# Kernel optimization log

Measured on AMD Instinct MI355X. Metric: run time of the kernel, lower is better.

## Reference

```python
import jax, jax.numpy as jnp
import numpy as np

K = 20  # n_neighbors

def _edge_features(x, k):
    # x: [B, C, N] -> edge features [B, 2C, N, k] using dynamic kNN graph
    sq = jnp.sum(x * x, axis=1)                          # [B, N]
    inner = jnp.einsum('bcn,bcm->bnm', x, x)             # [B, N, N]
    neg_dist = 2.0 * inner - sq[:, :, None] - sq[:, None, :]
    idx = jax.lax.top_k(neg_dist, k)[1]                  # [B, N, k] nearest neighbors
    # gather neighbor features: xj[b,c,n,j] = x[b,c,idx[b,n,j]]
    xj = jnp.take_along_axis(x[:, :, None, :], idx[:, None, :, :], axis=3)  # [B, C, N, k]
    xi = jnp.broadcast_to(x[:, :, :, None], xj.shape)
    return jnp.concatenate([xj - xi, xi], axis=1)        # [B, 2C, N, k]

def _lrelu(v):
    return jax.nn.leaky_relu(v, 0.2)

def _edge_conv(x, W, b, k):
    f = _edge_features(x, k)                              # [B, 2C, N, k]
    h = jnp.einsum('bcnk,oc->bonk', f, W) + b[None, :, None, None]
    return jnp.max(_lrelu(h), axis=3)                     # [B, O, N]

def setup_inputs() -> dict:
    key = jax.random.key(0)
    ks = jax.random.split(key, 12)
    conv_dims = (64, 64, 128, 256)
    in_dims = (3, 64, 64, 128)
    inp = {'x': jax.random.normal(ks[0], (16, 2048, 3), dtype=jnp.float32)}
    for i, (ci, co) in enumerate(zip(in_dims, conv_dims)):
        s = 1.0 / np.sqrt(2 * ci)
        inp[f'W{i}'] = jax.random.uniform(ks[1 + 2 * i], (co, 2 * ci), jnp.float32, -s, s)
        inp[f'b{i}'] = jax.random.uniform(ks[2 + 2 * i], (co,), jnp.float32, -s, s)
    sf = 1.0 / np.sqrt(sum(conv_dims))
    inp['Wf'] = jax.random.uniform(ks[9], (1024, sum(conv_dims)), jnp.float32, -sf, sf)
    inp['bf'] = jax.random.uniform(ks[10], (1024,), jnp.float32, -sf, sf)
    return inp

def reference(x, W0, b0, W1, b1, W2, b2, W3, b3, Wf, bf):
    h = jnp.transpose(x, (0, 2, 1))                       # [B, 3, N]
    xs = []
    for W, b in ((W0, b0), (W1, b1), (W2, b2), (W3, b3)):
        h = _edge_conv(h, W, b, K)
        xs.append(h)
    h = jnp.concatenate(xs, axis=1)                       # [B, 512, N]
    h = _lrelu(jnp.einsum('bcn,oc->bon', h, Wf) + bf[None, :, None])  # [B, 1024, N]
    return jnp.max(h, axis=2)                             # [B, 1024]
```

## Files before the change

kernel.cpp:

```cpp
#include <hip/hip_runtime.h>
#include <hip/hip_bf16.h>
#include <math.h>

#define NPTS 2048
#define NB 16
#define KNN 20

typedef __attribute__((ext_vector_type(8))) short bf16x8;
typedef __attribute__((ext_vector_type(4))) float f32x4;

__device__ __forceinline__ float lrelu(float v) { return fmaxf(v, 0.2f * v); }

__device__ __forceinline__ void split2(float a, float b, unsigned& hp, unsigned& lp) {
    float2 f2; f2.x = a; f2.y = b;
    __hip_bfloat162 h2 = __float22bfloat162_rn(f2);
    unsigned hb; __builtin_memcpy(&hb, &h2, 4);
    float la = a - __uint_as_float(hb << 16);
    float lb = b - __uint_as_float(hb & 0xFFFF0000u);
    float2 l2; l2.x = la; l2.y = lb;
    __hip_bfloat162 k2 = __float22bfloat162_rn(l2);
    unsigned lb2; __builtin_memcpy(&lb2, &k2, 4);
    hp = hb; lp = lb2;
}

template<int CTRL, int RM>
__device__ __forceinline__ float dpp_fmax_step(float x) {
    int t = __builtin_amdgcn_update_dpp((int)0xFF800000, __float_as_int(x),
                                        CTRL, RM, 0xF, false);
    return fmaxf(x, __int_as_float(t));
}
__device__ __forceinline__ float wave_max_bcast(float x) {
    x = dpp_fmax_step<0x111, 0xF>(x);
    x = dpp_fmax_step<0x112, 0xF>(x);
    x = dpp_fmax_step<0x114, 0xF>(x);
    x = dpp_fmax_step<0x118, 0xF>(x);
    x = dpp_fmax_step<0x142, 0xA>(x);
    x = dpp_fmax_step<0x143, 0xC>(x);
    return __int_as_float(__builtin_amdgcn_readlane(__float_as_int(x), 63));
}

__global__ void transpose_kernel(const float* __restrict__ x, float* __restrict__ h0) {
    int t = blockIdx.x * blockDim.x + threadIdx.x;
    if (t >= NB * NPTS) return;
    int b = t / NPTS, n = t % NPTS;
    const float* src = x + (size_t)t * 3;
    float* dst = h0 + (size_t)b * 3 * NPTS + n;
    dst[0]        = src[0];
    dst[NPTS]     = src[1];
    dst[2 * NPTS] = src[2];
}

template<int C>
__global__ __launch_bounds__(512) void knn_kernel(const float* __restrict__ xin, long bstride,
                                                  int* __restrict__ idx) {
    __shared__ __align__(16) float dist[8][NPTS];
    int b = blockIdx.y;
    int n0 = blockIdx.x * 8;
    int tid = threadIdx.x;
    const float* xb = xin + (size_t)b * bstride;
    const float* xq = xb + n0;

    int m0 = 4 * tid;
    float4 acc[8];
#pragma unroll
    for (int r = 0; r < 8; ++r) acc[r] = make_float4(0.f, 0.f, 0.f, 0.f);
    float4 sn = make_float4(0.f, 0.f, 0.f, 0.f);

#pragma unroll 4
    for (int c = 0; c < C; ++c) {
        const float* rowc = xb + (size_t)c * NPTS;
        float4 xv = *reinterpret_cast<const float4*>(&rowc[m0]);
        float4 q0 = *reinterpret_cast<const float4*>(&xq[(size_t)c * NPTS]);
        float4 q1 = *reinterpret_cast<const float4*>(&xq[(size_t)c * NPTS + 4]);
        sn.x = fmaf(xv.x, xv.x, sn.x);
        sn.y = fmaf(xv.y, xv.y, sn.y);
        sn.z = fmaf(xv.z, xv.z, sn.z);
        sn.w = fmaf(xv.w, xv.w, sn.w);
        float q[8] = {q0.x, q0.y, q0.z, q0.w, q1.x, q1.y, q1.z, q1.w};
#pragma unroll
        for (int r = 0; r < 8; ++r) {
            acc[r].x = fmaf(q[r], xv.x, acc[r].x);
            acc[r].y = fmaf(q[r], xv.y, acc[r].y);
            acc[r].z = fmaf(q[r], xv.z, acc[r].z);
            acc[r].w = fmaf(q[r], xv.w, acc[r].w);
        }
    }
    {
        int p = m0 ^ (((m0 >> 5) & 7) << 2);
#pragma unroll
        for (int r = 0; r < 8; ++r) {
            float4 dv;
            dv.x = 2.f * acc[r].x - sn.x;
            dv.y = 2.f * acc[r].y - sn.y;
            dv.z = 2.f * acc[r].z - sn.z;
            dv.w = 2.f * acc[r].w - sn.w;
            *reinterpret_cast<float4*>(&dist[r][p]) = dv;
        }
    }
    __syncthreads();

    int w = tid >> 6;
    int lane = tid & 63;
    float v[32];
    {
        const float* drow = &dist[w][32 * lane];
        int s = (lane & 7) << 2;
#pragma unroll
        for (int u = 0; u < 8; ++u) {
            float4 t = *reinterpret_cast<const float4*>(&drow[(4 * u) ^ s]);
            v[4 * u + 0] = t.x; v[4 * u + 1] = t.y;
            v[4 * u + 2] = t.z; v[4 * u + 3] = t.w;
        }
    }

    float gm[4]; int gi[4];
#pragma unroll
    for (int g = 0; g < 4; ++g) {
        gm[g] = v[8 * g]; gi[g] = 8 * g;
#pragma unroll
        for (int i = 1; i < 8; ++i)
            if (v[8 * g + i] > gm[g]) { gm[g] = v[8 * g + i]; gi[g] = 8 * g + i; }
    }
    float lv = gm[0]; int lm = gi[0];
#pragma unroll
    for (int g = 1; g < 4; ++g) if (gm[g] > lv) { lv = gm[g]; lm = gi[g]; }

    int rbm = 0;
    int* out = idx + ((size_t)b * NPTS + n0 + w) * KNN;

    for (int j = 0; j < KNN; ++j) {
        float gv = wave_max_bcast(lv);
        unsigned long long mk = __ballot(lv == gv);
        int winner = (int)__builtin_ctzll(mk);
        int wm = __builtin_amdgcn_readlane(lm, winner);
        int bm = winner * 32 + wm;
        rbm = (lane == j) ? bm : rbm;

        bool iswin = (lane == winner);
        int g = wm >> 3, ii = wm & 7;
#pragma unroll
        for (int gq = 0; gq < 4; ++gq) {
            if (gq == g) {
#pragma unroll
                for (int i = 0; i < 8; ++i)
                    v[8 * gq + i] = (iswin && (ii == i)) ? -INFINITY : v[8 * gq + i];
                float nm = v[8 * gq]; int ni = 8 * gq;
#pragma unroll
                for (int i = 1; i < 8; ++i)
                    if (v[8 * gq + i] > nm) { nm = v[8 * gq + i]; ni = 8 * gq + i; }
                gm[gq] = iswin ? nm : gm[gq];
                gi[gq] = iswin ? ni : gi[gq];
            }
        }
        lv = gm[0]; lm = gi[0];
#pragma unroll
        for (int g2 = 1; g2 < 4; ++g2) if (gm[g2] > lv) { lv = gm[g2]; lm = gi[g2]; }
    }
    if (lane < KNN) out[lane] = rbm;
}

__global__ void prep_w_kernel(const float* __restrict__ W, int C, int O,
                              float* __restrict__ Wa, float* __restrict__ Wd) {
    int t = blockIdx.x * blockDim.x + threadIdx.x;
    if (t >= C * O) return;
    int c = t / O, o = t % O;
    float a = W[o * 2 * C + c];
    float d = W[o * 2 * C + C + c] - a;
    Wa[c * O + o] = a;
    Wd[c * O + o] = d;
}

__global__ __launch_bounds__(256) void edge_mm_kernel(const float* __restrict__ xin, long bstride,
                                                      int C, int O,
                                                      const float* __restrict__ Wa,
                                                      const float* __restrict__ Wd,
                                                      const float* __restrict__ bias,
                                                      float* __restrict__ y,
                                                      float* __restrict__ base, long base_bstride) {
    int m = blockIdx.x * 256 + threadIdx.x;
    int ngrp = O >> 3;
    int og = blockIdx.y % ngrp, b = blockIdx.y / ngrp;
    int o0 = og * 8;
    const float* xb = xin + (size_t)b * bstride + m;
    float a1[8], a2[8];
#pragma unroll
    for (int i = 0; i < 8; ++i) { a1[i] = 0.f; a2[i] = 0.f; }
#pragma unroll 2
    for (int c = 0; c < C; ++c) {
        float h = xb[(size_t)c * NPTS];
        const float* wa = Wa + c * O + o0;
        const float* wd = Wd + c * O + o0;
#pragma unroll
        for (int i = 0; i < 8; ++i) {
            a1[i] = fmaf(wa[i], h, a1[i]);
            a2[i] = fmaf(wd[i], h, a2[i]);
        }
    }
#pragma unroll
    for (int i = 0; i < 8; ++i) {
        y[((size_t)b * O + o0 + i) * NPTS + m] = a1[i];
        base[(size_t)b * base_bstride + (size_t)(o0 + i) * NPTS + m] = a2[i] + bias[o0 + i];
    }
}

__global__ __launch_bounds__(256) void gather_max_kernel(const float* __restrict__ y, int O,
                                                         const int* __restrict__ idx,
                                                         float* __restrict__ feat_slice,
                                                         long bstride) {
    __shared__ float yrow[NPTS];
    int o = blockIdx.x, b = blockIdx.y;
    const float* ysrc = y + ((size_t)b * O + o) * NPTS;
    for (int m = threadIdx.x; m < NPTS; m += 256) yrow[m] = ysrc[m];
    __syncthreads();
    float* fs = feat_slice + (size_t)b * bstride + (size_t)o * NPTS;
    const int* ib = idx + (size_t)b * NPTS * KNN;
    for (int s = 0; s < 8; ++s) {
        int n = threadIdx.x + 256 * s;
        const int* ip = ib + n * KNN;
        float mx = -INFINITY;
#pragma unroll
        for (int j = 0; j < KNN; ++j) mx = fmaxf(mx, yrow[ip[j]]);
        fs[n] = lrelu(mx + fs[n]);
    }
}

__global__ void wf_split_kernel(const float* __restrict__ Wf,
                                unsigned* __restrict__ Wfh, unsigned* __restrict__ Wfl) {
    int t = blockIdx.x * 256 + threadIdx.x;
    if (t >= 262144) return;
    unsigned h, l;
    split2(Wf[2 * t], Wf[2 * t + 1], h, l);
    Wfh[t] = h; Wfl[t] = l;
}

#define GP 40
__global__ __launch_bounds__(256) void final_gemm_mfma(
    const float* __restrict__ feat,
    const unsigned short* __restrict__ Wfh,
    const unsigned short* __restrict__ Wfl,
    float* __restrict__ pmax) {
    __shared__ __align__(16) unsigned short Ah[128 * GP];
    __shared__ __align__(16) unsigned short Al[128 * GP];
    __shared__ __align__(16) unsigned short Bh[128 * GP];
    __shared__ __align__(16) unsigned short Bl[128 * GP];

    int ot = blockIdx.x, nt = blockIdx.y, b = blockIdx.z;
    int o0 = ot * 128, n0 = nt * 128;
    int tid = threadIdx.x;
    int lane = tid & 63, w = tid >> 6;
    int wm = w & 1, wn = w >> 1;
    int l15 = lane & 15, q = lane >> 4;

    f32x4 acc[4][4];
#pragma unroll
    for (int mi = 0; mi < 4; ++mi)
#pragma unroll
        for (int ni = 0; ni < 4; ++ni) acc[mi][ni] = (f32x4)0.f;

    const float* fb = feat + (size_t)b * 512 * NPTS;

    int bn = tid & 127, kh = tid >> 7;

    for (int c0 = 0; c0 < 512; c0 += 32) {
#pragma unroll
        for (int p = 0; p < 2; ++p) {
            int e = p * 256 + tid;
            int r = e >> 2, qq = e & 3;
            size_t go = (size_t)(o0 + r) * 512 + c0 + qq * 8;
            *(uint4*)&Ah[r * GP + qq * 8] = *(const uint4*)(Wfh + go);
            *(uint4*)&Al[r * GP + qq * 8] = *(const uint4*)(Wfl + go);
        }
        {
            const float* src = fb + (size_t)(c0 + kh * 16) * NPTS + n0 + bn;
            float v[16];
#pragma unroll
            for (int j = 0; j < 16; ++j) v[j] = src[(size_t)j * NPTS];
            unsigned hw[8], lw[8];
#pragma unroll
            for (int p = 0; p < 8; ++p) split2(v[2 * p], v[2 * p + 1], hw[p], lw[p]);
            unsigned short* bh = &Bh[bn * GP + kh * 16];
            unsigned short* bl = &Bl[bn * GP + kh * 16];
            *(uint4*)(bh)     = make_uint4(hw[0], hw[1], hw[2], hw[3]);
            *(uint4*)(bh + 8) = make_uint4(hw[4], hw[5], hw[6], hw[7]);
            *(uint4*)(bl)     = make_uint4(lw[0], lw[1], lw[2], lw[3]);
            *(uint4*)(bl + 8) = make_uint4(lw[4], lw[5], lw[6], lw[7]);
        }
        __syncthreads();

        bf16x8 bhf[4], blf[4];
#pragma unroll
        for (int ni = 0; ni < 4; ++ni) {
            int row = wn * 64 + ni * 16 + l15;
            bhf[ni] = *(const bf16x8*)&Bh[row * GP + q * 8];
            blf[ni] = *(const bf16x8*)&Bl[row * GP + q * 8];
        }
#pragma unroll
        for (int mi = 0; mi < 4; ++mi) {
            int row = wm * 64 + mi * 16 + l15;
            bf16x8 ah = *(const bf16x8*)&Ah[row * GP + q * 8];
            bf16x8 al = *(const bf16x8*)&Al[row * GP + q * 8];
#pragma unroll
            for (int ni = 0; ni < 4; ++ni) {
                acc[mi][ni] = __builtin_amdgcn_mfma_f32_16x16x32_bf16(ah, bhf[ni], acc[mi][ni], 0, 0, 0);
                acc[mi][ni] = __builtin_amdgcn_mfma_f32_16x16x32_bf16(ah, blf[ni], acc[mi][ni], 0, 0, 0);
                acc[mi][ni] = __builtin_amdgcn_mfma_f32_16x16x32_bf16(al, bhf[ni], acc[mi][ni], 0, 0, 0);
            }
        }
        __syncthreads();
    }

    int slot = nt * 2 + wn;
#pragma unroll
    for (int mi = 0; mi < 4; ++mi) {
        float m4[4];
#pragma unroll
        for (int r = 0; r < 4; ++r) {
            float m = acc[mi][0][r];
            m = fmaxf(m, acc[mi][1][r]);
            m = fmaxf(m, acc[mi][2][r]);
            m = fmaxf(m, acc[mi][3][r]);
            m4[r] = m;
        }
#pragma unroll
        for (int off = 1; off < 16; off <<= 1) {
#pragma unroll
            for (int r = 0; r < 4; ++r)
                m4[r] = fmaxf(m4[r], __shfl_xor(m4[r], off, 16));
        }
        if (l15 == 0) {
            int mbase = o0 + wm * 64 + mi * 16 + q * 4;
#pragma unroll
            for (int r = 0; r < 4; ++r)
                pmax[((size_t)b * 1024 + mbase + r) * 32 + slot] = m4[r];
        }
    }
}

__global__ void final_reduce_kernel(const float* __restrict__ pmax,
                                    const float* __restrict__ bf,
                                    float* __restrict__ out) {
    int t = blockIdx.x * blockDim.x + threadIdx.x;
    if (t >= NB * 1024) return;
    const float* p = pmax + (size_t)t * 32;
    float m = p[0];
#pragma unroll
    for (int i = 1; i < 32; ++i) m = fmaxf(m, p[i]);
    out[t] = lrelu(m + bf[t & 1023]);
}

extern "C" void kernel_launch(void* const* d_in, const int* in_sizes, int n_in,
                              void* d_out, int out_size, void* d_ws, size_t ws_size,
                              hipStream_t stream) {
    const float* x  = (const float*)d_in[0];
    const float* W[4]  = {(const float*)d_in[1], (const float*)d_in[3],
                          (const float*)d_in[5], (const float*)d_in[7]};
    const float* bb[4] = {(const float*)d_in[2], (const float*)d_in[4],
                          (const float*)d_in[6], (const float*)d_in[8]};
    const float* Wf = (const float*)d_in[9];
    const float* bf = (const float*)d_in[10];
    float* out = (float*)d_out;

    float* ws   = (float*)d_ws;
    float* h0   = ws;
    int*   idx  = (int*)(ws + 98304 + 32768);
    float* y    = (float*)(idx + 655360);
    float* feat = y + 8388608;
    float* Wa   = feat + 16777216 + 262144;
    float* Wd   = Wa + 32768;

    unsigned* Wfh = (unsigned*)y;
    unsigned* Wfl = (unsigned*)(y + 262144);
    float*    pmax = y + 524288;

    transpose_kernel<<<128, 256, 0, stream>>>(x, h0);

    const int  Cs[4]   = {3, 64, 64, 128};
    const int  Os[4]   = {64, 64, 128, 256};
    const int  offs[4] = {0, 64, 128, 256};

    for (int l = 0; l < 4; ++l) {
        const float* in = (l == 0) ? h0 : feat + (size_t)offs[l - 1] * NPTS;
        long bstr = (l == 0) ? (long)3 * NPTS : (long)512 * NPTS;
        int C = Cs[l], O = Os[l];

        dim3 kg(NPTS / 8, NB);
        if (C == 3)       knn_kernel<3>  <<<kg, 512, 0, stream>>>(in, bstr, idx);
        else if (C == 64) knn_kernel<64> <<<kg, 512, 0, stream>>>(in, bstr, idx);
        else              knn_kernel<128><<<kg, 512, 0, stream>>>(in, bstr, idx);

        prep_w_kernel<<<(C * O + 255) / 256, 256, 0, stream>>>(W[l], C, O, Wa, Wd);

        float* fslice = feat + (size_t)offs[l] * NPTS;
        edge_mm_kernel<<<dim3(NPTS / 256, NB * (O >> 3)), 256, 0, stream>>>(
            in, bstr, C, O, Wa, Wd, bb[l], y, fslice, (long)512 * NPTS);

        gather_max_kernel<<<dim3(O, NB), 256, 0, stream>>>(y, O, idx, fslice, (long)512 * NPTS);
    }

    wf_split_kernel<<<1024, 256, 0, stream>>>(Wf, Wfh, Wfl);
    final_gemm_mfma<<<dim3(8, 16, NB), 256, 0, stream>>>(
        feat, (const unsigned short*)Wfh, (const unsigned short*)Wfl, pmax);
    final_reduce_kernel<<<64, 256, 0, stream>>>(pmax, bf, out);
}
```

Before: 1.154 ms.

## Transpose kNN index layout and shrink kNN blocks to four query rows

The kNN kernel now uses 256-thread blocks that each handle 4 query points, with every thread computing 8 candidate distances instead of 4. Neighbor indices are stored transposed as [B, K, N] rather than [B, N, K]. With that layout, the gather-max kernel's per-neighbor index loads are coalesced across threads instead of strided by K. The smaller blocks halve shared memory per block and double the grid size, but reload the candidate rows twice as often per query.

```diff
diff --git a/kernel.cpp b/kernel.cpp
--- a/kernel.cpp
+++ b/kernel.cpp
@@ -51,50 +51,69 @@
 }
 
 template<int C>
-__global__ __launch_bounds__(512) void knn_kernel(const float* __restrict__ xin, long bstride,
-                                                  int* __restrict__ idx) {
-    __shared__ __align__(16) float dist[8][NPTS];
+__global__ __launch_bounds__(256) void knn_kernel(const float* __restrict__ xin, long bstride,
+                                                  int* __restrict__ idxT) {
+    __shared__ __align__(16) float dist[4][NPTS];
     int b = blockIdx.y;
-    int n0 = blockIdx.x * 8;
+    int n0 = blockIdx.x * 4;
     int tid = threadIdx.x;
     const float* xb = xin + (size_t)b * bstride;
     const float* xq = xb + n0;
 
-    int m0 = 4 * tid;
-    float4 acc[8];
-#pragma unroll
-    for (int r = 0; r < 8; ++r) acc[r] = make_float4(0.f, 0.f, 0.f, 0.f);
-    float4 sn = make_float4(0.f, 0.f, 0.f, 0.f);
+    int m0 = 8 * tid;
+    float4 acc[4][2];
+#pragma unroll
+    for (int r = 0; r < 4; ++r)
+#pragma unroll
+        for (int h = 0; h < 2; ++h) acc[r][h] = make_float4(0.f, 0.f, 0.f, 0.f);
+    float4 sn[2];
+    sn[0] = make_float4(0.f, 0.f, 0.f, 0.f);
+    sn[1] = make_float4(0.f, 0.f, 0.f, 0.f);
 
 #pragma unroll 4
     for (int c = 0; c < C; ++c) {
         const float* rowc = xb + (size_t)c * NPTS;
-        float4 xv = *reinterpret_cast<const float4*>(&rowc[m0]);
-        float4 q0 = *reinterpret_cast<const float4*>(&xq[(size_t)c * NPTS]);
-        float4 q1 = *reinterpret_cast<const float4*>(&xq[(size_t)c * NPTS + 4]);
-        sn.x = fmaf(xv.x, xv.x, sn.x);
-        sn.y = fmaf(xv.y, xv.y, sn.y);
-        sn.z = fmaf(xv.z, xv.z, sn.z);
-        sn.w = fmaf(xv.w, xv.w, sn.w);
-        float q[8] = {q0.x, q0.y, q0.z, q0.w, q1.x, q1.y, q1.z, q1.w};
-#pragma unroll
-        for (int r = 0; r < 8; ++r) {
-            acc[r].x = fmaf(q[r], xv.x, acc[r].x);
-            acc[r].y = fmaf(q[r], xv.y, acc[r].y);
-            acc[r].z = fmaf(q[r], xv.z, acc[r].z);
-            acc[r].w = fmaf(q[r], xv.w, acc[r].w);
+        float4 xv0 = *reinterpret_cast<const float4*>(&rowc[m0]);
+        float4 xv1 = *reinterpret_cast<const float4*>(&rowc[m0 + 4]);
+        float4 qv  = *reinterpret_cast<const float4*>(&xq[(size_t)c * NPTS]);
+        sn[0].x = fmaf(xv0.x, xv0.x, sn[0].x);
+        sn[0].y = fmaf(xv0.y, xv0.y, sn[0].y);
+        sn[0].z = fmaf(xv0.z, xv0.z, sn[0].z);
+        sn[0].w = fmaf(xv0.w, xv0.w, sn[0].w);
+        sn[1].x = fmaf(xv1.x, xv1.x, sn[1].x);
+        sn[1].y = fmaf(xv1.y, xv1.y, sn[1].y);
+        sn[1].z = fmaf(xv1.z, xv1.z, sn[1].z);
+        sn[1].w = fmaf(xv1.w, xv1.w, sn[1].w);
+        float q[4] = {qv.x, qv.y, qv.z, qv.w};
+#pragma unroll
+        for (int r = 0; r < 4; ++r) {
+            acc[r][0].x = fmaf(q[r], xv0.x, acc[r][0].x);
+            acc[r][0].y = fmaf(q[r], xv0.y, acc[r][0].y);
+            acc[r][0].z = fmaf(q[r], xv0.z, acc[r][0].z);
+            acc[r][0].w = fmaf(q[r], xv0.w, acc[r][0].w);
+            acc[r][1].x = fmaf(q[r], xv1.x, acc[r][1].x);
+            acc[r][1].y = fmaf(q[r], xv1.y, acc[r][1].y);
+            acc[r][1].z = fmaf(q[r], xv1.z, acc[r][1].z);
+            acc[r][1].w = fmaf(q[r], xv1.w, acc[r][1].w);
         }
     }
     {
-        int p = m0 ^ (((m0 >> 5) & 7) << 2);
-#pragma unroll
-        for (int r = 0; r < 8; ++r) {
-            float4 dv;
-            dv.x = 2.f * acc[r].x - sn.x;
-            dv.y = 2.f * acc[r].y - sn.y;
-            dv.z = 2.f * acc[r].z - sn.z;
-            dv.w = 2.f * acc[r].w - sn.w;
-            *reinterpret_cast<float4*>(&dist[r][p]) = dv;
+        int sw = ((m0 >> 5) & 7) << 2;
+        int p0 = m0 ^ sw;
+        int p1 = (m0 + 4) ^ sw;
+#pragma unroll
+        for (int r = 0; r < 4; ++r) {
+            float4 d0, d1;
+            d0.x = 2.f * acc[r][0].x - sn[0].x;
+            d0.y = 2.f * acc[r][0].y - sn[0].y;
+            d0.z = 2.f * acc[r][0].z - sn[0].z;
+            d0.w = 2.f * acc[r][0].w - sn[0].w;
+            d1.x = 2.f * acc[r][1].x - sn[1].x;
+            d1.y = 2.f * acc[r][1].y - sn[1].y;
+            d1.z = 2.f * acc[r][1].z - sn[1].z;
+            d1.w = 2.f * acc[r][1].w - sn[1].w;
+            *reinterpret_cast<float4*>(&dist[r][p0]) = d0;
+            *reinterpret_cast<float4*>(&dist[r][p1]) = d1;
         }
     }
     __syncthreads();
@@ -126,7 +145,6 @@
     for (int g = 1; g < 4; ++g) if (gm[g] > lv) { lv = gm[g]; lm = gi[g]; }
 
     int rbm = 0;
-    int* out = idx + ((size_t)b * NPTS + n0 + w) * KNN;
 
     for (int j = 0; j < KNN; ++j) {
         float gv = wave_max_bcast(lv);
@@ -156,7 +174,7 @@
 #pragma unroll
         for (int g2 = 1; g2 < 4; ++g2) if (gm[g2] > lv) { lv = gm[g2]; lm = gi[g2]; }
     }
-    if (lane < KNN) out[lane] = rbm;
+    if (lane < KNN) idxT[((size_t)b * KNN + lane) * NPTS + n0 + w] = rbm;
 }
 
 __global__ void prep_w_kernel(const float* __restrict__ W, int C, int O,
@@ -204,7 +222,7 @@
 }
 
 __global__ __launch_bounds__(256) void gather_max_kernel(const float* __restrict__ y, int O,
-                                                         const int* __restrict__ idx,
+                                                         const int* __restrict__ idxT,
                                                          float* __restrict__ feat_slice,
                                                          long bstride) {
     __shared__ float yrow[NPTS];
@@ -213,13 +231,12 @@
     for (int m = threadIdx.x; m < NPTS; m += 256) yrow[m] = ysrc[m];
     __syncthreads();
     float* fs = feat_slice + (size_t)b * bstride + (size_t)o * NPTS;
-    const int* ib = idx + (size_t)b * NPTS * KNN;
+    const int* ib = idxT + (size_t)b * KNN * NPTS;
     for (int s = 0; s < 8; ++s) {
         int n = threadIdx.x + 256 * s;
-        const int* ip = ib + n * KNN;
         float mx = -INFINITY;
 #pragma unroll
-        for (int j = 0; j < KNN; ++j) mx = fmaxf(mx, yrow[ip[j]]);
+        for (int j = 0; j < KNN; ++j) mx = fmaxf(mx, yrow[ib[(size_t)j * NPTS + n]]);
         fs[n] = lrelu(mx + fs[n]);
     }
 }
@@ -362,8 +379,8 @@
 
     float* ws   = (float*)d_ws;
     float* h0   = ws;
-    int*   idx  = (int*)(ws + 98304 + 32768);
-    float* y    = (float*)(idx + 655360);
+    int*   idxT = (int*)(ws + 98304 + 32768);
+    float* y    = (float*)(idxT + 655360);
     float* feat = y + 8388608;
     float* Wa   = feat + 16777216 + 262144;
     float* Wd   = Wa + 32768;
@@ -383,10 +400,10 @@
         long bstr = (l == 0) ? (long)3 * NPTS : (long)512 * NPTS;
         int C = Cs[l], O = Os[l];
 
-        dim3 kg(NPTS / 8, NB);
-        if (C == 3)       knn_kernel<3>  <<<kg, 512, 0, stream>>>(in, bstr, idx);
-        else if (C == 64) knn_kernel<64> <<<kg, 512, 0, stream>>>(in, bstr, idx);
-        else              knn_kernel<128><<<kg, 512, 0, stream>>>(in, bstr, idx);
+        dim3 kg(NPTS / 4, NB);
+        if (C == 3)       knn_kernel<3>  <<<kg, 256, 0, stream>>>(in, bstr, idxT);
+        else if (C == 64) knn_kernel<64> <<<kg, 256, 0, stream>>>(in, bstr, idxT);
+        else              knn_kernel<128><<<kg, 256, 0, stream>>>(in, bstr, idxT);
 
         prep_w_kernel<<<(C * O + 255) / 256, 256, 0, stream>>>(W[l], C, O, Wa, Wd);
 
@@ -394,7 +411,7 @@
         edge_mm_kernel<<<dim3(NPTS / 256, NB * (O >> 3)), 256, 0, stream>>>(
             in, bstr, C, O, Wa, Wd, bb[l], y, fslice, (long)512 * NPTS);
 
-        gather_max_kernel<<<dim3(O, NB), 256, 0, stream>>>(y, O, idx, fslice, (long)512 * NPTS);
+        gather_max_kernel<<<dim3(O, NB), 256, 0, stream>>>(y, O, idxT, fslice, (long)512 * NPTS);
     }
 
     wf_split_kernel<<<1024, 256, 0, stream>>>(Wf, Wfh, Wfl);
```

Measured after the change: 1.236 ms. 1.07x slower.

## Compute kNN distances with bf16x3-split MFMA and two-pass top-k selection

Applied to the files above, without the earlier changes.

Replaces the FP32 FMA pairwise-distance kNN kernel with a pre-pass that splits each point's features into three bf16 parts plus squared norms, then a kernel that computes the inner products with six 16x16x32 bf16 MFMAs per chunk, recovering near-FP32 accuracy. Each block handles 16 query rows in two halves of 1024 candidates. It picks 20 candidates per half and merges them with a second wave-level selection. The index layout becomes transposed [B,K,N] so that gather_max reads are coalesced. This adds an extra split kernel and its memory traffic per layer, and the bf16 split could rarely change neighbor ordering on near ties.

```diff
diff --git a/kernel.cpp b/kernel.cpp
--- a/kernel.cpp
+++ b/kernel.cpp
@@ -10,6 +10,14 @@
 typedef __attribute__((ext_vector_type(4))) float f32x4;
 
 __device__ __forceinline__ float lrelu(float v) { return fmaxf(v, 0.2f * v); }
+
+__device__ __forceinline__ unsigned short bf16r(float a) {
+    __hip_bfloat16 h = __float2bfloat16(a);
+    unsigned short u; __builtin_memcpy(&u, &h, 2); return u;
+}
+__device__ __forceinline__ float bf2f(unsigned short u) {
+    unsigned v = (unsigned)u << 16; float f; __builtin_memcpy(&f, &v, 4); return f;
+}
 
 __device__ __forceinline__ void split2(float a, float b, unsigned& hp, unsigned& lp) {
     float2 f2; f2.x = a; f2.y = b;
@@ -50,113 +58,172 @@
     dst[2 * NPTS] = src[2];
 }
 
-template<int C>
-__global__ __launch_bounds__(512) void knn_kernel(const float* __restrict__ xin, long bstride,
-                                                  int* __restrict__ idx) {
-    __shared__ __align__(16) float dist[8][NPTS];
-    int b = blockIdx.y;
-    int n0 = blockIdx.x * 8;
-    int tid = threadIdx.x;
-    const float* xb = xin + (size_t)b * bstride;
-    const float* xq = xb + n0;
-
-    int m0 = 4 * tid;
-    float4 acc[8];
-#pragma unroll
-    for (int r = 0; r < 8; ++r) acc[r] = make_float4(0.f, 0.f, 0.f, 0.f);
-    float4 sn = make_float4(0.f, 0.f, 0.f, 0.f);
-
-#pragma unroll 4
-    for (int c = 0; c < C; ++c) {
-        const float* rowc = xb + (size_t)c * NPTS;
-        float4 xv = *reinterpret_cast<const float4*>(&rowc[m0]);
-        float4 q0 = *reinterpret_cast<const float4*>(&xq[(size_t)c * NPTS]);
-        float4 q1 = *reinterpret_cast<const float4*>(&xq[(size_t)c * NPTS + 4]);
-        sn.x = fmaf(xv.x, xv.x, sn.x);
-        sn.y = fmaf(xv.y, xv.y, sn.y);
-        sn.z = fmaf(xv.z, xv.z, sn.z);
-        sn.w = fmaf(xv.w, xv.w, sn.w);
-        float q[8] = {q0.x, q0.y, q0.z, q0.w, q1.x, q1.y, q1.z, q1.w};
-#pragma unroll
-        for (int r = 0; r < 8; ++r) {
-            acc[r].x = fmaf(q[r], xv.x, acc[r].x);
-            acc[r].y = fmaf(q[r], xv.y, acc[r].y);
-            acc[r].z = fmaf(q[r], xv.z, acc[r].z);
-            acc[r].w = fmaf(q[r], xv.w, acc[r].w);
-        }
-    }
+template<int C, int CP>
+__global__ __launch_bounds__(256) void split_sq_kernel(const float* __restrict__ in, long bstride,
+                                                       unsigned short* __restrict__ xs,
+                                                       float* __restrict__ sq) {
+    int t = blockIdx.x * 256 + threadIdx.x;
+    int b = t >> 11, n = t & 2047;
+    const float* p = in + (size_t)b * bstride + n;
+    unsigned short* o = xs + (size_t)t * 3 * CP;
+    float s = 0.f;
+    for (int c0 = 0; c0 < CP; c0 += 4) {
+        unsigned short hh[4], mm[4], ll[4];
+#pragma unroll
+        for (int i = 0; i < 4; ++i) {
+            int c = c0 + i;
+            float a = (c < C) ? p[(size_t)c * NPTS] : 0.f;
+            if (c < C) s = fmaf(a, a, s);
+            unsigned short h = bf16r(a);
+            float r1 = a - bf2f(h);
+            unsigned short m = bf16r(r1);
+            float r2 = r1 - bf2f(m);
+            unsigned short l = bf16r(r2);
+            hh[i] = h; mm[i] = m; ll[i] = l;
+        }
+        *(uint2*)(o + 0 * CP + c0) = make_uint2((unsigned)hh[0] | ((unsigned)hh[1] << 16),
+                                                (unsigned)hh[2] | ((unsigned)hh[3] << 16));
+        *(uint2*)(o + 1 * CP + c0) = make_uint2((unsigned)mm[0] | ((unsigned)mm[1] << 16),
+                                                (unsigned)mm[2] | ((unsigned)mm[3] << 16));
+        *(uint2*)(o + 2 * CP + c0) = make_uint2((unsigned)ll[0] | ((unsigned)ll[1] << 16),
+                                                (unsigned)ll[2] | ((unsigned)ll[3] << 16));
+    }
+    sq[t] = s;
+}
+
+template<int CP>
+__global__ __launch_bounds__(512) void knn_mfma_kernel(const unsigned short* __restrict__ xs,
+                                                       const float* __restrict__ sq,
+                                                       int* __restrict__ idxT) {
+    __shared__ __align__(16) float dist[16 * 1024];
+    constexpr int KC = CP / 32;
+    int b = blockIdx.y, n0 = blockIdx.x * 16;
+    int tid = threadIdx.x, lane = tid & 63, w = tid >> 6;
+    int l15 = lane & 15, q = lane >> 4;
+
+    bf16x8 af[KC][3];
     {
-        int p = m0 ^ (((m0 >> 5) & 7) << 2);
-#pragma unroll
-        for (int r = 0; r < 8; ++r) {
-            float4 dv;
-            dv.x = 2.f * acc[r].x - sn.x;
-            dv.y = 2.f * acc[r].y - sn.y;
-            dv.z = 2.f * acc[r].z - sn.z;
-            dv.w = 2.f * acc[r].w - sn.w;
-            *reinterpret_cast<float4*>(&dist[r][p]) = dv;
-        }
-    }
-    __syncthreads();
-
-    int w = tid >> 6;
-    int lane = tid & 63;
-    float v[32];
-    {
-        const float* drow = &dist[w][32 * lane];
-        int s = (lane & 7) << 2;
-#pragma unroll
-        for (int u = 0; u < 8; ++u) {
-            float4 t = *reinterpret_cast<const float4*>(&drow[(4 * u) ^ s]);
-            v[4 * u + 0] = t.x; v[4 * u + 1] = t.y;
-            v[4 * u + 2] = t.z; v[4 * u + 3] = t.w;
-        }
-    }
-
-    float gm[4]; int gi[4];
-#pragma unroll
-    for (int g = 0; g < 4; ++g) {
-        gm[g] = v[8 * g]; gi[g] = 8 * g;
-#pragma unroll
-        for (int i = 1; i < 8; ++i)
-            if (v[8 * g + i] > gm[g]) { gm[g] = v[8 * g + i]; gi[g] = 8 * g + i; }
-    }
-    float lv = gm[0]; int lm = gi[0];
-#pragma unroll
-    for (int g = 1; g < 4; ++g) if (gm[g] > lv) { lv = gm[g]; lm = gi[g]; }
-
-    int rbm = 0;
-    int* out = idx + ((size_t)b * NPTS + n0 + w) * KNN;
-
-    for (int j = 0; j < KNN; ++j) {
-        float gv = wave_max_bcast(lv);
-        unsigned long long mk = __ballot(lv == gv);
-        int winner = (int)__builtin_ctzll(mk);
-        int wm = __builtin_amdgcn_readlane(lm, winner);
-        int bm = winner * 32 + wm;
-        rbm = (lane == j) ? bm : rbm;
-
-        bool iswin = (lane == winner);
-        int g = wm >> 3, ii = wm & 7;
-#pragma unroll
-        for (int gq = 0; gq < 4; ++gq) {
-            if (gq == g) {
-#pragma unroll
-                for (int i = 0; i < 8; ++i)
-                    v[8 * gq + i] = (iswin && (ii == i)) ? -INFINITY : v[8 * gq + i];
-                float nm = v[8 * gq]; int ni = 8 * gq;
-#pragma unroll
-                for (int i = 1; i < 8; ++i)
-                    if (v[8 * gq + i] > nm) { nm = v[8 * gq + i]; ni = 8 * gq + i; }
-                gm[gq] = iswin ? nm : gm[gq];
-                gi[gq] = iswin ? ni : gi[gq];
-            }
-        }
-        lv = gm[0]; lm = gi[0];
-#pragma unroll
-        for (int g2 = 1; g2 < 4; ++g2) if (gm[g2] > lv) { lv = gm[g2]; lm = gi[g2]; }
-    }
-    if (lane < KNN) out[lane] = rbm;
+        const unsigned short* ab = xs + ((size_t)b * NPTS + n0 + l15) * 3 * CP + q * 8;
+#pragma unroll
+        for (int kc = 0; kc < KC; ++kc)
+#pragma unroll
+            for (int cp = 0; cp < 3; ++cp)
+                af[kc][cp] = *(const bf16x8*)(ab + (size_t)cp * CP + kc * 32);
+    }
+    const float* sqb = sq + (size_t)b * NPTS;
+
+    float avalr[2]; int aidxr[2];
+    avalr[0] = avalr[1] = 0.f; aidxr[0] = aidxr[1] = 0;
+
+    for (int half = 0; half < 2; ++half) {
+        int chalf = half * 1024;
+        int lcb0 = w * 128;
+#pragma unroll 2
+        for (int t8 = 0; t8 < 8; ++t8) {
+            int lcb = lcb0 + t8 * 16;
+            int gc = chalf + lcb + l15;
+            const unsigned short* bb = xs + ((size_t)b * NPTS + gc) * 3 * CP + q * 8;
+            f32x4 acc = (f32x4)0.f;
+#pragma unroll
+            for (int kc = 0; kc < KC; ++kc) {
+                bf16x8 bh = *(const bf16x8*)(bb + 0 * CP + kc * 32);
+                bf16x8 bm = *(const bf16x8*)(bb + 1 * CP + kc * 32);
+                bf16x8 bl = *(const bf16x8*)(bb + 2 * CP + kc * 32);
+                acc = __builtin_amdgcn_mfma_f32_16x16x32_bf16(af[kc][1], bm, acc, 0, 0, 0);
+                acc = __builtin_amdgcn_mfma_f32_16x16x32_bf16(af[kc][0], bl, acc, 0, 0, 0);
+                acc = __builtin_amdgcn_mfma_f32_16x16x32_bf16(af[kc][2], bh, acc, 0, 0, 0);
+                acc = __builtin_amdgcn_mfma_f32_16x16x32_bf16(af[kc][0], bm, acc, 0, 0, 0);
+                acc = __builtin_amdgcn_mfma_f32_16x16x32_bf16(af[kc][1], bh, acc, 0, 0, 0);
+                acc = __builtin_amdgcn_mfma_f32_16x16x32_bf16(af[kc][0], bh, acc, 0, 0, 0);
+            }
+            float sv = sqb[gc];
+            int lc = lcb + l15;
+            int pc = lc ^ (((lc >> 5) & 7) << 2);
+#pragma unroll
+            for (int j = 0; j < 4; ++j) {
+                int r = q * 4 + j;
+                dist[r * 1024 + ((pc + 4 * r) & 1023)] = 2.f * acc[j] - sv;
+            }
+        }
+        __syncthreads();
+
+        int swl = ((lane >> 1) & 7) << 2;
+        for (int rs = 0; rs < 2; ++rs) {
+            int r = w + 8 * rs;
+            float v[16];
+#pragma unroll
+            for (int u = 0; u < 4; ++u) {
+                int lcl = (16 * lane + 4 * u) ^ swl;
+                const float4 tv = *(const float4*)&dist[r * 1024 + ((lcl + 4 * r) & 1023)];
+                v[4 * u + 0] = tv.x; v[4 * u + 1] = tv.y;
+                v[4 * u + 2] = tv.z; v[4 * u + 3] = tv.w;
+            }
+            float gm0 = v[0]; int gi0 = 0;
+            float gm1 = v[8]; int gi1 = 8;
+#pragma unroll
+            for (int i = 1; i < 8; ++i) {
+                if (v[i] > gm0) { gm0 = v[i]; gi0 = i; }
+                if (v[8 + i] > gm1) { gm1 = v[8 + i]; gi1 = 8 + i; }
+            }
+            float lv = gm0; int lm = gi0;
+            if (gm1 > lv) { lv = gm1; lm = gi1; }
+
+            float cv = -INFINITY; int ci = 0;
+            for (int j = 0; j < KNN; ++j) {
+                float gv = wave_max_bcast(lv);
+                unsigned long long mk = __ballot(lv == gv);
+                int winner = (int)__builtin_ctzll(mk);
+                int wm = __builtin_amdgcn_readlane(lm, winner);
+                int bm = chalf + winner * 16 + wm;
+                cv = (lane == j) ? gv : cv;
+                ci = (lane == j) ? bm : ci;
+                bool iswin = (lane == winner);
+                if ((wm >> 3) == 0) {
+#pragma unroll
+                    for (int i = 0; i < 8; ++i)
+                        v[i] = (iswin && (wm == i)) ? -INFINITY : v[i];
+                    float nm = v[0]; int ni = 0;
+#pragma unroll
+                    for (int i = 1; i < 8; ++i) if (v[i] > nm) { nm = v[i]; ni = i; }
+                    gm0 = iswin ? nm : gm0;
+                    gi0 = iswin ? ni : gi0;
+                } else {
+#pragma unroll
+                    for (int i = 8; i < 16; ++i)
+                        v[i] = (iswin && (wm == i)) ? -INFINITY : v[i];
+                    float nm = v[8]; int ni = 8;
+#pragma unroll
+                    for (int i = 9; i < 16; ++i) if (v[i] > nm) { nm = v[i]; ni = i; }
+                    gm1 = iswin ? nm : gm1;
+                    gi1 = iswin ? ni : gi1;
+                }
+                lv = gm0; lm = gi0;
+                if (gm1 > lv) { lv = gm1; lm = gi1; }
+            }
+
+            if (half == 0) { avalr[rs] = cv; aidxr[rs] = ci; }
+            else {
+                int src = (lane >= 32) ? (lane - 32) : 0;
+                float bsv = __shfl(cv, src, 64);
+                int   bsi = __shfl(ci, src, 64);
+                float mv; int mi2;
+                if (lane < 20)                    { mv = avalr[rs]; mi2 = aidxr[rs]; }
+                else if (lane >= 32 && lane < 52) { mv = bsv;       mi2 = bsi; }
+                else                              { mv = -INFINITY; mi2 = 0; }
+                int rbm = 0;
+                for (int j = 0; j < KNN; ++j) {
+                    float gv = wave_max_bcast(mv);
+                    unsigned long long mk = __ballot(mv == gv);
+                    int winner = (int)__builtin_ctzll(mk);
+                    int widx = __builtin_amdgcn_readlane(mi2, winner);
+                    rbm = (lane == j) ? widx : rbm;
+                    mv = (lane == winner) ? -INFINITY : mv;
+                }
+                if (lane < KNN) idxT[((size_t)b * KNN + lane) * NPTS + n0 + r] = rbm;
+            }
+        }
+        if (half == 0) __syncthreads();
+    }
 }
 
 __global__ void prep_w_kernel(const float* __restrict__ W, int C, int O,
@@ -204,7 +271,7 @@
 }
 
 __global__ __launch_bounds__(256) void gather_max_kernel(const float* __restrict__ y, int O,
-                                                         const int* __restrict__ idx,
+                                                         const int* __restrict__ idxT,
                                                          float* __restrict__ feat_slice,
                                                          long bstride) {
     __shared__ float yrow[NPTS];
@@ -213,13 +280,12 @@
     for (int m = threadIdx.x; m < NPTS; m += 256) yrow[m] = ysrc[m];
     __syncthreads();
     float* fs = feat_slice + (size_t)b * bstride + (size_t)o * NPTS;
-    const int* ib = idx + (size_t)b * NPTS * KNN;
+    const int* ib = idxT + (size_t)b * KNN * NPTS;
     for (int s = 0; s < 8; ++s) {
         int n = threadIdx.x + 256 * s;
-        const int* ip = ib + n * KNN;
         float mx = -INFINITY;
 #pragma unroll
-        for (int j = 0; j < KNN; ++j) mx = fmaxf(mx, yrow[ip[j]]);
+        for (int j = 0; j < KNN; ++j) mx = fmaxf(mx, yrow[ib[(size_t)j * NPTS + n]]);
         fs[n] = lrelu(mx + fs[n]);
     }
 }
@@ -258,7 +324,6 @@
         for (int ni = 0; ni < 4; ++ni) acc[mi][ni] = (f32x4)0.f;
 
     const float* fb = feat + (size_t)b * 512 * NPTS;
-
     int bn = tid & 127, kh = tid >> 7;
 
     for (int c0 = 0; c0 < 512; c0 += 32) {
@@ -362,11 +427,14 @@
 
     float* ws   = (float*)d_ws;
     float* h0   = ws;
-    int*   idx  = (int*)(ws + 98304 + 32768);
-    float* y    = (float*)(idx + 655360);
+    float* sq   = ws + 98304;
+    int*   idxT = (int*)(sq + 32768);
+    float* y    = (float*)(idxT + 655360);
     float* feat = y + 8388608;
     float* Wa   = feat + 16777216 + 262144;
     float* Wd   = Wa + 32768;
+
+    unsigned short* xs = (unsigned short*)y;
 
     unsigned* Wfh = (unsigned*)y;
     unsigned* Wfl = (unsigned*)(y + 262144);
@@ -383,10 +451,17 @@
         long bstr = (l == 0) ? (long)3 * NPTS : (long)512 * NPTS;
         int C = Cs[l], O = Os[l];
 
-        dim3 kg(NPTS / 8, NB);
-        if (C == 3)       knn_kernel<3>  <<<kg, 512, 0, stream>>>(in, bstr, idx);
-        else if (C == 64) knn_kernel<64> <<<kg, 512, 0, stream>>>(in, bstr, idx);
-        else              knn_kernel<128><<<kg, 512, 0, stream>>>(in, bstr, idx);
+        dim3 kg(NPTS / 16, NB);
+        if (C == 3) {
+            split_sq_kernel<3, 32><<<128, 256, 0, stream>>>(in, bstr, xs, sq);
+            knn_mfma_kernel<32><<<kg, 512, 0, stream>>>(xs, sq, idxT);
+        } else if (C == 64) {
+            split_sq_kernel<64, 64><<<128, 256, 0, stream>>>(in, bstr, xs, sq);
+            knn_mfma_kernel<64><<<kg, 512, 0, stream>>>(xs, sq, idxT);
+        } else {
+            split_sq_kernel<128, 128><<<128, 256, 0, stream>>>(in, bstr, xs, sq);
+            knn_mfma_kernel<128><<<kg, 512, 0, stream>>>(xs, sq, idxT);
+        }
 
         prep_w_kernel<<<(C * O + 255) / 256, 256, 0, stream>>>(W[l], C, O, Wa, Wd);
 
@@ -394,7 +469,7 @@
         edge_mm_kernel<<<dim3(NPTS / 256, NB * (O >> 3)), 256, 0, stream>>>(
             in, bstr, C, O, Wa, Wd, bb[l], y, fslice, (long)512 * NPTS);
 
-        gather_max_kernel<<<dim3(O, NB), 256, 0, stream>>>(y, O, idx, fslice, (long)512 * NPTS);
+        gather_max_kernel<<<dim3(O, NB), 256, 0, stream>>>(y, O, idxT, fslice, (long)512 * NPTS);
     }
 
     wf_split_kernel<<<1024, 256, 0, stream>>>(Wf, Wfh, Wfl);
```

Result: slower. 1.747 ms (+51.4%).

## Transpose kNN index layout and process two query groups per kNN block

Applied to the files above, without the earlier changes.

The kNN index buffer is stored transposed as [B, K, N], so the gather-max kernel reads indices coalesced across threads instead of with a stride of K per thread. Each kNN block now handles 16 query points in two sequential rounds of 8, halving the grid and reusing the block's shared distance buffer. The doubled work per block adds an extra barrier and serialises the two rounds, so fewer blocks are available to hide latency. The idx writes from the kNN kernel become scattered across N-strided rows.

```diff
diff --git a/kernel.cpp b/kernel.cpp
--- a/kernel.cpp
+++ b/kernel.cpp
@@ -52,111 +52,114 @@
 
 template<int C>
 __global__ __launch_bounds__(512) void knn_kernel(const float* __restrict__ xin, long bstride,
-                                                  int* __restrict__ idx) {
+                                                  int* __restrict__ idxT) {
     __shared__ __align__(16) float dist[8][NPTS];
     int b = blockIdx.y;
-    int n0 = blockIdx.x * 8;
     int tid = threadIdx.x;
+    int lane = tid & 63, w = tid >> 6;
     const float* xb = xin + (size_t)b * bstride;
-    const float* xq = xb + n0;
-
     int m0 = 4 * tid;
-    float4 acc[8];
-#pragma unroll
-    for (int r = 0; r < 8; ++r) acc[r] = make_float4(0.f, 0.f, 0.f, 0.f);
-    float4 sn = make_float4(0.f, 0.f, 0.f, 0.f);
+
+    for (int rg = 0; rg < 2; ++rg) {
+        int n0 = blockIdx.x * 16 + rg * 8;
+        const float* xq = xb + n0;
+
+        float4 acc[8];
+#pragma unroll
+        for (int r = 0; r < 8; ++r) acc[r] = make_float4(0.f, 0.f, 0.f, 0.f);
+        float4 sn = make_float4(0.f, 0.f, 0.f, 0.f);
 
 #pragma unroll 4
-    for (int c = 0; c < C; ++c) {
-        const float* rowc = xb + (size_t)c * NPTS;
-        float4 xv = *reinterpret_cast<const float4*>(&rowc[m0]);
-        float4 q0 = *reinterpret_cast<const float4*>(&xq[(size_t)c * NPTS]);
-        float4 q1 = *reinterpret_cast<const float4*>(&xq[(size_t)c * NPTS + 4]);
-        sn.x = fmaf(xv.x, xv.x, sn.x);
-        sn.y = fmaf(xv.y, xv.y, sn.y);
-        sn.z = fmaf(xv.z, xv.z, sn.z);
-        sn.w = fmaf(xv.w, xv.w, sn.w);
-        float q[8] = {q0.x, q0.y, q0.z, q0.w, q1.x, q1.y, q1.z, q1.w};
-#pragma unroll
-        for (int r = 0; r < 8; ++r) {
-            acc[r].x = fmaf(q[r], xv.x, acc[r].x);
-            acc[r].y = fmaf(q[r], xv.y, acc[r].y);
-            acc[r].z = fmaf(q[r], xv.z, acc[r].z);
-            acc[r].w = fmaf(q[r], xv.w, acc[r].w);
-        }
-    }
-    {
-        int p = m0 ^ (((m0 >> 5) & 7) << 2);
-#pragma unroll
-        for (int r = 0; r < 8; ++r) {
-            float4 dv;
-            dv.x = 2.f * acc[r].x - sn.x;
-            dv.y = 2.f * acc[r].y - sn.y;
-            dv.z = 2.f * acc[r].z - sn.z;
-            dv.w = 2.f * acc[r].w - sn.w;
-            *reinterpret_cast<float4*>(&dist[r][p]) = dv;
-        }
-    }
-    __syncthreads();
-
-    int w = tid >> 6;
-    int lane = tid & 63;
-    float v[32];
-    {
-        const float* drow = &dist[w][32 * lane];
-        int s = (lane & 7) << 2;
-#pragma unroll
-        for (int u = 0; u < 8; ++u) {
-            float4 t = *reinterpret_cast<const float4*>(&drow[(4 * u) ^ s]);
-            v[4 * u + 0] = t.x; v[4 * u + 1] = t.y;
-            v[4 * u + 2] = t.z; v[4 * u + 3] = t.w;
-        }
-    }
-
-    float gm[4]; int gi[4];
-#pragma unroll
-    for (int g = 0; g < 4; ++g) {
-        gm[g] = v[8 * g]; gi[g] = 8 * g;
-#pragma unroll
-        for (int i = 1; i < 8; ++i)
-            if (v[8 * g + i] > gm[g]) { gm[g] = v[8 * g + i]; gi[g] = 8 * g + i; }
-    }
-    float lv = gm[0]; int lm = gi[0];
-#pragma unroll
-    for (int g = 1; g < 4; ++g) if (gm[g] > lv) { lv = gm[g]; lm = gi[g]; }
-
-    int rbm = 0;
-    int* out = idx + ((size_t)b * NPTS + n0 + w) * KNN;
-
-    for (int j = 0; j < KNN; ++j) {
-        float gv = wave_max_bcast(lv);
-        unsigned long long mk = __ballot(lv == gv);
-        int winner = (int)__builtin_ctzll(mk);
-        int wm = __builtin_amdgcn_readlane(lm, winner);
-        int bm = winner * 32 + wm;
-        rbm = (lane == j) ? bm : rbm;
-
-        bool iswin = (lane == winner);
-        int g = wm >> 3, ii = wm & 7;
-#pragma unroll
-        for (int gq = 0; gq < 4; ++gq) {
-            if (gq == g) {
-#pragma unroll
-                for (int i = 0; i < 8; ++i)
-                    v[8 * gq + i] = (iswin && (ii == i)) ? -INFINITY : v[8 * gq + i];
-                float nm = v[8 * gq]; int ni = 8 * gq;
-#pragma unroll
-                for (int i = 1; i < 8; ++i)
-                    if (v[8 * gq + i] > nm) { nm = v[8 * gq + i]; ni = 8 * gq + i; }
-                gm[gq] = iswin ? nm : gm[gq];
-                gi[gq] = iswin ? ni : gi[gq];
+        for (int c = 0; c < C; ++c) {
+            const float* rowc = xb + (size_t)c * NPTS;
+            float4 xv = *reinterpret_cast<const float4*>(&rowc[m0]);
+            float4 q0 = *reinterpret_cast<const float4*>(&xq[(size_t)c * NPTS]);
+            float4 q1 = *reinterpret_cast<const float4*>(&xq[(size_t)c * NPTS + 4]);
+            sn.x = fmaf(xv.x, xv.x, sn.x);
+            sn.y = fmaf(xv.y, xv.y, sn.y);
+            sn.z = fmaf(xv.z, xv.z, sn.z);
+            sn.w = fmaf(xv.w, xv.w, sn.w);
+            float q[8] = {q0.x, q0.y, q0.z, q0.w, q1.x, q1.y, q1.z, q1.w};
+#pragma unroll
+            for (int r = 0; r < 8; ++r) {
+                acc[r].x = fmaf(q[r], xv.x, acc[r].x);
+                acc[r].y = fmaf(q[r], xv.y, acc[r].y);
+                acc[r].z = fmaf(q[r], xv.z, acc[r].z);
+                acc[r].w = fmaf(q[r], xv.w, acc[r].w);
             }
         }
-        lv = gm[0]; lm = gi[0];
-#pragma unroll
-        for (int g2 = 1; g2 < 4; ++g2) if (gm[g2] > lv) { lv = gm[g2]; lm = gi[g2]; }
-    }
-    if (lane < KNN) out[lane] = rbm;
+        {
+            int p = m0 ^ (((m0 >> 5) & 7) << 2);
+#pragma unroll
+            for (int r = 0; r < 8; ++r) {
+                float4 dv;
+                dv.x = 2.f * acc[r].x - sn.x;
+                dv.y = 2.f * acc[r].y - sn.y;
+                dv.z = 2.f * acc[r].z - sn.z;
+                dv.w = 2.f * acc[r].w - sn.w;
+                *reinterpret_cast<float4*>(&dist[r][p]) = dv;
+            }
+        }
+        __syncthreads();
+
+        float v[32];
+        {
+            const float* drow = &dist[w][32 * lane];
+            int s = (lane & 7) << 2;
+#pragma unroll
+            for (int u = 0; u < 8; ++u) {
+                float4 t = *reinterpret_cast<const float4*>(&drow[(4 * u) ^ s]);
+                v[4 * u + 0] = t.x; v[4 * u + 1] = t.y;
+                v[4 * u + 2] = t.z; v[4 * u + 3] = t.w;
+            }
+        }
+
+        float gm[4]; int gi[4];
+#pragma unroll
+        for (int g = 0; g < 4; ++g) {
+            gm[g] = v[8 * g]; gi[g] = 8 * g;
+#pragma unroll
+            for (int i = 1; i < 8; ++i)
+                if (v[8 * g + i] > gm[g]) { gm[g] = v[8 * g + i]; gi[g] = 8 * g + i; }
+        }
+        float lv = gm[0]; int lm = gi[0];
+#pragma unroll
+        for (int g = 1; g < 4; ++g) if (gm[g] > lv) { lv = gm[g]; lm = gi[g]; }
+
+        int rbm = 0;
+
+        for (int j = 0; j < KNN; ++j) {
+            float gv = wave_max_bcast(lv);
+            unsigned long long mk = __ballot(lv == gv);
+            int winner = (int)__builtin_ctzll(mk);
+            int wm = __builtin_amdgcn_readlane(lm, winner);
+            int bm = winner * 32 + wm;
+            rbm = (lane == j) ? bm : rbm;
+
+            bool iswin = (lane == winner);
+            int g = wm >> 3, ii = wm & 7;
+#pragma unroll
+            for (int gq = 0; gq < 4; ++gq) {
+                if (gq == g) {
+#pragma unroll
+                    for (int i = 0; i < 8; ++i)
+                        v[8 * gq + i] = (iswin && (ii == i)) ? -INFINITY : v[8 * gq + i];
+                    float nm = v[8 * gq]; int ni = 8 * gq;
+#pragma unroll
+                    for (int i = 1; i < 8; ++i)
+                        if (v[8 * gq + i] > nm) { nm = v[8 * gq + i]; ni = 8 * gq + i; }
+                    gm[gq] = iswin ? nm : gm[gq];
+                    gi[gq] = iswin ? ni : gi[gq];
+                }
+            }
+            lv = gm[0]; lm = gi[0];
+#pragma unroll
+            for (int g2 = 1; g2 < 4; ++g2) if (gm[g2] > lv) { lv = gm[g2]; lm = gi[g2]; }
+        }
+        if (lane < KNN) idxT[((size_t)b * KNN + lane) * NPTS + n0 + w] = rbm;
+
+        if (rg == 0) __syncthreads();
+    }
 }
 
 __global__ void prep_w_kernel(const float* __restrict__ W, int C, int O,
@@ -204,7 +207,7 @@
 }
 
 __global__ __launch_bounds__(256) void gather_max_kernel(const float* __restrict__ y, int O,
-                                                         const int* __restrict__ idx,
+                                                         const int* __restrict__ idxT,
                                                          float* __restrict__ feat_slice,
                                                          long bstride) {
     __shared__ float yrow[NPTS];
@@ -213,13 +216,12 @@
     for (int m = threadIdx.x; m < NPTS; m += 256) yrow[m] = ysrc[m];
     __syncthreads();
     float* fs = feat_slice + (size_t)b * bstride + (size_t)o * NPTS;
-    const int* ib = idx + (size_t)b * NPTS * KNN;
+    const int* ib = idxT + (size_t)b * KNN * NPTS;
     for (int s = 0; s < 8; ++s) {
         int n = threadIdx.x + 256 * s;
-        const int* ip = ib + n * KNN;
         float mx = -INFINITY;
 #pragma unroll
-        for (int j = 0; j < KNN; ++j) mx = fmaxf(mx, yrow[ip[j]]);
+        for (int j = 0; j < KNN; ++j) mx = fmaxf(mx, yrow[ib[(size_t)j * NPTS + n]]);
         fs[n] = lrelu(mx + fs[n]);
     }
 }
@@ -258,7 +260,6 @@
         for (int ni = 0; ni < 4; ++ni) acc[mi][ni] = (f32x4)0.f;
 
     const float* fb = feat + (size_t)b * 512 * NPTS;
-
     int bn = tid & 127, kh = tid >> 7;
 
     for (int c0 = 0; c0 < 512; c0 += 32) {
@@ -362,8 +363,8 @@
 
     float* ws   = (float*)d_ws;
     float* h0   = ws;
-    int*   idx  = (int*)(ws + 98304 + 32768);
-    float* y    = (float*)(idx + 655360);
+    int*   idxT = (int*)(ws + 98304 + 32768);
+    float* y    = (float*)(idxT + 655360);
     float* feat = y + 8388608;
     float* Wa   = feat + 16777216 + 262144;
     float* Wd   = Wa + 32768;
@@ -383,10 +384,10 @@
         long bstr = (l == 0) ? (long)3 * NPTS : (long)512 * NPTS;
         int C = Cs[l], O = Os[l];
 
-        dim3 kg(NPTS / 8, NB);
-        if (C == 3)       knn_kernel<3>  <<<kg, 512, 0, stream>>>(in, bstr, idx);
-        else if (C == 64) knn_kernel<64> <<<kg, 512, 0, stream>>>(in, bstr, idx);
-        else              knn_kernel<128><<<kg, 512, 0, stream>>>(in, bstr, idx);
+        dim3 kg(NPTS / 16, NB);
+        if (C == 3)       knn_kernel<3>  <<<kg, 512, 0, stream>>>(in, bstr, idxT);
+        else if (C == 64) knn_kernel<64> <<<kg, 512, 0, stream>>>(in, bstr, idxT);
+        else              knn_kernel<128><<<kg, 512, 0, stream>>>(in, bstr, idxT);
 
         prep_w_kernel<<<(C * O + 255) / 256, 256, 0, stream>>>(W[l], C, O, Wa, Wd);
 
@@ -394,7 +395,7 @@
         edge_mm_kernel<<<dim3(NPTS / 256, NB * (O >> 3)), 256, 0, stream>>>(
             in, bstr, C, O, Wa, Wd, bb[l], y, fslice, (long)512 * NPTS);
 
-        gather_max_kernel<<<dim3(O, NB), 256, 0, stream>>>(y, O, idx, fslice, (long)512 * NPTS);
+        gather_max_kernel<<<dim3(O, NB), 256, 0, stream>>>(y, O, idxT, fslice, (long)512 * NPTS);
     }
 
     wf_split_kernel<<<1024, 256, 0, stream>>>(Wf, Wfh, Wfl);
```

Result: faster. 1.124 ms (-2.6%).
